# Kernel tuning notes

Hardware: AMD Instinct MI355X
Metric: run time of the kernel (lower is better)

Reference implementation:

```python
import jax, jax.numpy as jnp
import numpy as np

N = 50000      # nodes
DEG = 16       # fixed neighbor count per node -> E = N*DEG edges
F_IN = 128
F_OUT = 128


def setup_inputs() -> dict:
    key = jax.random.key(0)
    k = jax.random.split(key, 6)
    E = N * DEG
    x = jax.random.normal(k[0], (N, F_IN), dtype=jnp.float32)
    weight = jax.random.normal(k[1], (F_IN, F_OUT), dtype=jnp.float32) * (1.0 / np.sqrt(F_OUT))
    bias = jax.random.normal(k[2], (F_OUT,), dtype=jnp.float32) * (1.0 / np.sqrt(F_OUT))
    weights_mask = jax.random.normal(k[3], (2 * F_IN, F_IN), dtype=jnp.float32) * (1.0 / np.sqrt(F_IN))
    adj_vals = jax.random.uniform(k[4], (E,), dtype=jnp.float32)
    edge_src = jax.random.randint(k[5], (E,), 0, N, dtype=jnp.int32)   # neighbor ids (add_all flattened)
    edge_dst = jnp.repeat(jnp.arange(N, dtype=jnp.int32), DEG)         # center node ids
    return {"x": x, "weight": weight, "bias": bias, "weights_mask": weights_mask,
            "adj_vals": adj_vals, "edge_src": edge_src, "edge_dst": edge_dst}


def reference(x, weight, bias, weights_mask, adj_vals, edge_src, edge_dst):
    # Per-edge: concat(center, neighbor) -> mask MLP -> sigmoid (dropout omitted: eval mode)
    cen = x[edge_dst]                    # [E, F]
    nei = x[edge_src]                    # [E, F]
    cen_nei = jnp.concatenate([cen, nei], axis=1)          # [E, 2F]
    mask = jax.nn.sigmoid(cen_nei @ weights_mask)          # [E, F]
    # Weighted neighbor sum scattered back to centers, plus self feature
    agg = jax.ops.segment_sum(mask * nei, edge_dst, num_segments=N)   # [N, F]
    x_new = x + agg
    # Dense transform then spmm aggregation (adj given as edge list with values)
    support = x_new @ weight                                # [N, F_out]
    out = jax.ops.segment_sum(adj_vals[:, None] * support[edge_src], edge_dst, num_segments=N)
    return out + bias
```

## Files before the change

### kernel.cpp

```cpp
#include <hip/hip_runtime.h>
#include <stdint.h>
#include <stddef.h>


#define NNODES 50000
#define DEG    16
#define FD     128

#define NEG_LOG2E -1.44269504f

typedef __bf16 bf16x8 __attribute__((ext_vector_type(8)));
typedef short  s16x8  __attribute__((ext_vector_type(8)));
typedef float  f32x4  __attribute__((ext_vector_type(4)));
typedef float  f32x2  __attribute__((ext_vector_type(2)));

__device__ __forceinline__ short f2bf_s(float f) {
    union { float f; uint32_t u; } v; v.f = f;
    uint32_t r = v.u + 0x7fffu + ((v.u >> 16) & 1u);
    return (short)(r >> 16);
}
__device__ __forceinline__ float bflo(uint32_t u) {
    union { uint32_t u; float f; } v; v.u = u << 16;
    return v.f;
}
__device__ __forceinline__ float bfhi(uint32_t u) {
    union { uint32_t u; float f; } v; v.u = u & 0xffff0000u;
    return v.f;
}

__global__ __launch_bounds__(256) void pack_k(const float* __restrict__ wm,
                                              const float* __restrict__ w,
                                              short* __restrict__ wmb,
                                              short* __restrict__ wpack) {
    int tid = blockIdx.x * 256 + threadIdx.x;
    if (tid < 128 * 256) {
        int k = tid >> 8, c = tid & 255;
        float v = (c < 128) ? wm[k * 128 + c] : wm[(128 + k) * 128 + (c - 128)];
        int idx = (((k >> 5) * 16 + (c >> 4)) * 64 + ((k >> 3) & 3) * 16 + (c & 15)) * 8 + (k & 7);
        wmb[idx] = f2bf_s(NEG_LOG2E * v);
    }
    if (tid < 128 * 128) {
        int k = tid >> 7, n = tid & 127;
        int idx = (((k >> 5) * 8 + (n >> 4)) * 64 + ((k >> 3) & 3) * 16 + (n & 15)) * 8 + (k & 7);
        wpack[idx] = f2bf_s(w[tid]);
    }
}

__global__ __launch_bounds__(256) void zy_k(const float* __restrict__ x,
                                            const short* __restrict__ wmb,
                                            short* __restrict__ zbf,
                                            uint32_t* __restrict__ xy) {
    __shared__ float ct[16 * 260];
    const int tid = threadIdx.x, wave = tid >> 6, lane = tid & 63;
    const int q = lane >> 4, m = lane & 15;
    const int node0 = blockIdx.x * 16;

    f32x4 acc[4];
    #pragma unroll
    for (int nt = 0; nt < 4; ++nt) acc[nt] = (f32x4){0.f, 0.f, 0.f, 0.f};

    #pragma unroll
    for (int kk = 0; kk < 4; ++kk) {
        const float* rp = x + (size_t)(node0 + m) * FD + kk * 32 + q * 8;
        f32x4 lo = *reinterpret_cast<const f32x4*>(rp);
        f32x4 hi = *reinterpret_cast<const f32x4*>(rp + 4);
        bf16x8 a;
        a[0]=(__bf16)lo.x; a[1]=(__bf16)lo.y; a[2]=(__bf16)lo.z; a[3]=(__bf16)lo.w;
        a[4]=(__bf16)hi.x; a[5]=(__bf16)hi.y; a[6]=(__bf16)hi.z; a[7]=(__bf16)hi.w;
        #pragma unroll
        for (int nt = 0; nt < 4; ++nt) {
            int frag = kk * 16 + wave * 4 + nt;
            s16x8 braw = *reinterpret_cast<const s16x8*>(wmb + ((size_t)frag * 64 + lane) * 8);
            acc[nt] = __builtin_amdgcn_mfma_f32_16x16x32_bf16(a, __builtin_bit_cast(bf16x8, braw), acc[nt], 0, 0, 0);
        }
    }
    #pragma unroll
    for (int nt = 0; nt < 4; ++nt)
        #pragma unroll
        for (int i = 0; i < 4; ++i)
            ct[(q * 4 + i) * 260 + wave * 64 + nt * 16 + m] = acc[nt][i];
    __syncthreads();

    const int row = tid >> 4;
    const int c0  = (tid & 15) * 16;
    const int grow = node0 + row;
    if (c0 < 128) {
        uint32_t zo[8];
        #pragma unroll
        for (int j = 0; j < 8; ++j) {
            float v0 = ct[row * 260 + c0 + 2 * j];
            float v1 = ct[row * 260 + c0 + 2 * j + 1];
            zo[j] = (uint32_t)(uint16_t)f2bf_s(v0) | ((uint32_t)(uint16_t)f2bf_s(v1) << 16);
        }
        uint4* dst = reinterpret_cast<uint4*>(zbf + (size_t)grow * FD + c0);
        dst[0] = make_uint4(zo[0], zo[1], zo[2], zo[3]);
        dst[1] = make_uint4(zo[4], zo[5], zo[6], zo[7]);
    } else {
        const int f0 = c0 - 128;
        const float* xr = x + (size_t)grow * FD + f0;
        uint4* dst = reinterpret_cast<uint4*>(xy + (size_t)grow * FD + f0);
        #pragma unroll
        for (int v = 0; v < 4; ++v) {
            uint32_t xo[4];
            #pragma unroll
            for (int j = 0; j < 4; ++j) {
                float yv = ct[row * 260 + c0 + v * 4 + j];
                float xv = xr[v * 4 + j];
                xo[j] = (uint32_t)(uint16_t)f2bf_s(xv) | ((uint32_t)(uint16_t)f2bf_s(yv) << 16);
            }
            dst[v] = make_uint4(xo[0], xo[1], xo[2], xo[3]);
        }
    }
}

__global__ __launch_bounds__(256) void edge_k(const short* __restrict__ zbf,
                                              const uint32_t* __restrict__ xy,
                                              const int* __restrict__ esrc,
                                              const short* __restrict__ wpack,
                                              short* __restrict__ support) {
    __shared__ float xn[16 * 132];
    const int tid = threadIdx.x, wave = tid >> 6, lane = tid & 63;
    const int q = lane >> 4, m = lane & 15;
    const int node0 = blockIdx.x * 16;
    const int nu0 = __builtin_amdgcn_readfirstlane(node0 + wave * 4);

    uint2     buf[2][16];
    uint2     cr[2];
    uint32_t  zr[2];

    {
        const int* ep = esrc + nu0 * DEG;
        #pragma unroll
        for (int e = 0; e < 16; ++e)
            buf[0][e] = reinterpret_cast<const uint2*>(xy + (size_t)ep[e] * FD)[lane];
        zr[0] = reinterpret_cast<const uint32_t*>(zbf + (size_t)nu0 * FD)[lane];
        cr[0] = reinterpret_cast<const uint2*>(xy + (size_t)nu0 * FD)[lane];
    }

    #pragma unroll
    for (int mt = 0; mt < 4; ++mt) {
        const int cur = mt & 1, nxt = cur ^ 1;
        if (mt < 3) {
            const int nun = nu0 + mt + 1;
            const int* ep = esrc + nun * DEG;
            #pragma unroll
            for (int e = 0; e < 16; ++e)
                buf[nxt][e] = reinterpret_cast<const uint2*>(xy + (size_t)ep[e] * FD)[lane];
            zr[nxt] = reinterpret_cast<const uint32_t*>(zbf + (size_t)nun * FD)[lane];
            cr[nxt] = reinterpret_cast<const uint2*>(xy + (size_t)nun * FD)[lane];
        }
        const float zn0 = bflo(zr[cur]), zn1 = bfhi(zr[cur]);
        float a0a = 0.f, a0b = 0.f, a1a = 0.f, a1b = 0.f;
        #pragma unroll
        for (int e = 0; e < 16; ++e) {
            uint2 u = buf[cur][e];
            float g0 = __builtin_amdgcn_rcpf(1.f + __builtin_amdgcn_exp2f(zn0 + bfhi(u.x)));
            float g1 = __builtin_amdgcn_rcpf(1.f + __builtin_amdgcn_exp2f(zn1 + bfhi(u.y)));
            if (e & 1) { a0b += g0 * bflo(u.x); a1b += g1 * bflo(u.y); }
            else       { a0a += g0 * bflo(u.x); a1a += g1 * bflo(u.y); }
        }
        f32x2 xv;
        xv.x = bflo(cr[cur].x) + a0a + a0b;
        xv.y = bflo(cr[cur].y) + a1a + a1b;
        *reinterpret_cast<f32x2*>(&xn[(wave * 4 + mt) * 132 + 2 * lane]) = xv;
    }
    __syncthreads();

    f32x4 sacc[2];
    sacc[0] = (f32x4){0.f, 0.f, 0.f, 0.f};
    sacc[1] = (f32x4){0.f, 0.f, 0.f, 0.f};
    #pragma unroll
    for (int kk = 0; kk < 4; ++kk) {
        const float* p = &xn[m * 132 + kk * 32 + q * 8];
        bf16x8 a;
        a[0]=(__bf16)p[0]; a[1]=(__bf16)p[1]; a[2]=(__bf16)p[2]; a[3]=(__bf16)p[3];
        a[4]=(__bf16)p[4]; a[5]=(__bf16)p[5]; a[6]=(__bf16)p[6]; a[7]=(__bf16)p[7];
        #pragma unroll
        for (int t = 0; t < 2; ++t) {
            int nt = wave * 2 + t;
            s16x8 braw = *reinterpret_cast<const s16x8*>(wpack + ((size_t)(kk * 8 + nt) * 64 + lane) * 8);
            sacc[t] = __builtin_amdgcn_mfma_f32_16x16x32_bf16(a, __builtin_bit_cast(bf16x8, braw), sacc[t], 0, 0, 0);
        }
    }
    #pragma unroll
    for (int t = 0; t < 2; ++t) {
        int nt = wave * 2 + t;
        #pragma unroll
        for (int i = 0; i < 4; ++i)
            support[(size_t)(node0 + q * 4 + i) * FD + nt * 16 + m] = f2bf_s(sacc[t][i]);
    }
}

__global__ __launch_bounds__(256) void final_k(const short* __restrict__ support,
                                               const float* __restrict__ adj,
                                               const int* __restrict__ esrc,
                                               const float* __restrict__ bias,
                                               float* __restrict__ out) {
    const int tid = threadIdx.x, wave = tid >> 6, lane = tid & 63;
    const int n0 = blockIdx.x * 16 + wave * 4;
    f32x2 b = *reinterpret_cast<const f32x2*>(bias + 2 * lane);

    int nu[4];
    const int* ep[4];
    const float* ap[4];
    #pragma unroll
    for (int t = 0; t < 4; ++t) {
        nu[t] = __builtin_amdgcn_readfirstlane(n0 + t);
        ep[t] = esrc + nu[t] * DEG;
        ap[t] = adj + nu[t] * DEG;
    }
    float a0[4], a1[4];
    #pragma unroll
    for (int t = 0; t < 4; ++t) { a0[t] = b.x; a1[t] = b.y; }

    #pragma unroll
    for (int e = 0; e < 16; ++e) {
        #pragma unroll
        for (int t = 0; t < 4; ++t) {
            int s = ep[t][e];
            float w = ap[t][e];
            uint32_t u = reinterpret_cast<const uint32_t*>(support + (size_t)s * FD)[lane];
            a0[t] += w * bflo(u);
            a1[t] += w * bfhi(u);
        }
    }
    #pragma unroll
    for (int t = 0; t < 4; ++t) {
        f32x2 r; r.x = a0[t]; r.y = a1[t];
        *reinterpret_cast<f32x2*>(out + (size_t)nu[t] * FD + 2 * lane) = r;
    }
}

extern "C" void kernel_launch(void* const* d_in, const int* in_sizes, int n_in,
                              void* d_out, int out_size, void* d_ws, size_t ws_size,
                              hipStream_t stream) {
    const float* x      = (const float*)d_in[0];
    const float* weight = (const float*)d_in[1];
    const float* bias   = (const float*)d_in[2];
    const float* wm     = (const float*)d_in[3];
    const float* adj    = (const float*)d_in[4];
    const int*   esrc   = (const int*)d_in[5];

    short*    wmb     = (short*)d_ws;
    short*    wpack   = (short*)((char*)d_ws + 65536);
    short*    zbf     = (short*)((char*)d_ws + 98304);
    short*    support = (short*)((char*)d_ws + 98304 + (size_t)NNODES * FD * 2);
    uint32_t* xy      = (uint32_t*)d_out;
    float*    out     = (float*)d_out;

    pack_k <<<128,         256, 0, stream>>>(wm, weight, wmb, wpack);
    zy_k   <<<NNODES / 16, 256, 0, stream>>>(x, wmb, zbf, xy);
    edge_k <<<NNODES / 16, 256, 0, stream>>>(zbf, xy, esrc, wpack, support);
    final_k<<<NNODES / 16, 256, 0, stream>>>(support, adj, esrc, bias, out);
}
```

Baseline: 198.1 us.

## Reorder spmm before weight GEMM, store neighbor mask term in fp8

Uses linearity to aggregate x_new over neighbors first and apply the weight matrix afterwards, so the GEMM is fused into the final aggregation kernel and the intermediate support tensor disappears. The edge kernel now writes bf16 x_new and drops the in-kernel GEMM and LDS staging. The neighbor-side mask projection y is stored as fp8 in a separate array from the bf16 x, which cuts the bytes gathered per edge. Risks are lower precision in the mask logits and the extra rounding of x_new to bf16 before aggregation.

```diff
diff --git a/kernel.cpp b/kernel.cpp
--- a/kernel.cpp
+++ b/kernel.cpp
@@ -49,7 +49,8 @@
 __global__ __launch_bounds__(256) void zy_k(const float* __restrict__ x,
                                             const short* __restrict__ wmb,
                                             short* __restrict__ zbf,
-                                            uint32_t* __restrict__ xy) {
+                                            uint32_t* __restrict__ xb,
+                                            uint8_t* __restrict__ y8) {
     __shared__ float ct[16 * 260];
     const int tid = threadIdx.x, wave = tid >> 6, lane = tid & 63;
     const int q = lane >> 4, m = lane & 15;
@@ -98,71 +99,110 @@
     } else {
         const int f0 = c0 - 128;
         const float* xr = x + (size_t)grow * FD + f0;
-        uint4* dst = reinterpret_cast<uint4*>(xy + (size_t)grow * FD + f0);
-        #pragma unroll
-        for (int v = 0; v < 4; ++v) {
-            uint32_t xo[4];
-            #pragma unroll
-            for (int j = 0; j < 4; ++j) {
-                float yv = ct[row * 260 + c0 + v * 4 + j];
-                float xv = xr[v * 4 + j];
-                xo[j] = (uint32_t)(uint16_t)f2bf_s(xv) | ((uint32_t)(uint16_t)f2bf_s(yv) << 16);
-            }
-            dst[v] = make_uint4(xo[0], xo[1], xo[2], xo[3]);
-        }
+        uint32_t xo[8];
+        #pragma unroll
+        for (int j = 0; j < 8; ++j) {
+            float v0 = xr[2 * j], v1 = xr[2 * j + 1];
+            xo[j] = (uint32_t)(uint16_t)f2bf_s(v0) | ((uint32_t)(uint16_t)f2bf_s(v1) << 16);
+        }
+        uint4* xdst = reinterpret_cast<uint4*>(xb + (size_t)grow * 64 + f0 / 2);
+        xdst[0] = make_uint4(xo[0], xo[1], xo[2], xo[3]);
+        xdst[1] = make_uint4(xo[4], xo[5], xo[6], xo[7]);
+        uint32_t yo[4];
+        #pragma unroll
+        for (int g = 0; g < 4; ++g) {
+            float y0 = ct[row * 260 + c0 + 4 * g];
+            float y1 = ct[row * 260 + c0 + 4 * g + 1];
+            float y2 = ct[row * 260 + c0 + 4 * g + 2];
+            float y3 = ct[row * 260 + c0 + 4 * g + 3];
+            int u = __builtin_amdgcn_cvt_pk_fp8_f32(y0, y1, 0, false);
+            u     = __builtin_amdgcn_cvt_pk_fp8_f32(y2, y3, u, true);
+            yo[g] = (uint32_t)u;
+        }
+        *reinterpret_cast<uint4*>(y8 + (size_t)grow * 128 + f0) = make_uint4(yo[0], yo[1], yo[2], yo[3]);
     }
 }
 
 __global__ __launch_bounds__(256) void edge_k(const short* __restrict__ zbf,
-                                              const uint32_t* __restrict__ xy,
+                                              const uint32_t* __restrict__ xb,
+                                              const uint8_t* __restrict__ y8,
                                               const int* __restrict__ esrc,
-                                              const short* __restrict__ wpack,
-                                              short* __restrict__ support) {
+                                              uint32_t* __restrict__ xnb) {
+    const int tid = threadIdx.x, wave = tid >> 6, lane = tid & 63;
+    const int wn0 = blockIdx.x * 16 + wave * 4;
+
+    #pragma unroll
+    for (int pr = 0; pr < 2; ++pr) {
+        const int nuA = __builtin_amdgcn_readfirstlane(wn0 + pr * 2);
+        const int nuB = __builtin_amdgcn_readfirstlane(wn0 + pr * 2 + 1);
+        const int* epA = esrc + nuA * DEG;
+        const int* epB = esrc + nuB * DEG;
+        uint32_t zA = reinterpret_cast<const uint32_t*>(zbf + (size_t)nuA * FD)[lane];
+        uint32_t zB = reinterpret_cast<const uint32_t*>(zbf + (size_t)nuB * FD)[lane];
+        uint32_t cAw = xb[(size_t)nuA * 64 + lane];
+        uint32_t cBw = xb[(size_t)nuB * 64 + lane];
+        const float zA0 = bflo(zA), zA1 = bfhi(zA);
+        const float zB0 = bflo(zB), zB1 = bfhi(zB);
+        float aA0 = 0.f, aA1 = 0.f, bA0 = 0.f, bA1 = 0.f;
+        float aB0 = 0.f, aB1 = 0.f, bB0 = 0.f, bB1 = 0.f;
+        #pragma unroll
+        for (int e = 0; e < 16; ++e) {
+            const int sA = epA[e], sB = epB[e];
+            uint32_t xA = xb[(size_t)sA * 64 + lane];
+            uint32_t xB = xb[(size_t)sB * 64 + lane];
+            uint32_t yA = *reinterpret_cast<const uint16_t*>(y8 + (size_t)sA * 128 + 2 * lane);
+            uint32_t yB = *reinterpret_cast<const uint16_t*>(y8 + (size_t)sB * 128 + 2 * lane);
+            f32x2 pA = __builtin_amdgcn_cvt_pk_f32_fp8((int)yA, false);
+            f32x2 pB = __builtin_amdgcn_cvt_pk_f32_fp8((int)yB, false);
+            float gA0 = __builtin_amdgcn_rcpf(1.f + __builtin_amdgcn_exp2f(zA0 + pA.x));
+            float gA1 = __builtin_amdgcn_rcpf(1.f + __builtin_amdgcn_exp2f(zA1 + pA.y));
+            float gB0 = __builtin_amdgcn_rcpf(1.f + __builtin_amdgcn_exp2f(zB0 + pB.x));
+            float gB1 = __builtin_amdgcn_rcpf(1.f + __builtin_amdgcn_exp2f(zB1 + pB.y));
+            if (e & 1) { bA0 += gA0 * bflo(xA); bA1 += gA1 * bfhi(xA); bB0 += gB0 * bflo(xB); bB1 += gB1 * bfhi(xB); }
+            else       { aA0 += gA0 * bflo(xA); aA1 += gA1 * bfhi(xA); aB0 += gB0 * bflo(xB); aB1 += gB1 * bfhi(xB); }
+        }
+        float xA0 = bflo(cAw) + aA0 + bA0, xA1 = bfhi(cAw) + aA1 + bA1;
+        float xB0 = bflo(cBw) + aB0 + bB0, xB1 = bfhi(cBw) + aB1 + bB1;
+        xnb[(size_t)nuA * 64 + lane] = (uint32_t)(uint16_t)f2bf_s(xA0) | ((uint32_t)(uint16_t)f2bf_s(xA1) << 16);
+        xnb[(size_t)nuB * 64 + lane] = (uint32_t)(uint16_t)f2bf_s(xB0) | ((uint32_t)(uint16_t)f2bf_s(xB1) << 16);
+    }
+}
+
+__global__ __launch_bounds__(256) void out_k(const uint32_t* __restrict__ xnb,
+                                             const float* __restrict__ adj,
+                                             const int* __restrict__ esrc,
+                                             const short* __restrict__ wpack,
+                                             const float* __restrict__ bias,
+                                             float* __restrict__ out) {
     __shared__ float xn[16 * 132];
     const int tid = threadIdx.x, wave = tid >> 6, lane = tid & 63;
     const int q = lane >> 4, m = lane & 15;
     const int node0 = blockIdx.x * 16;
-    const int nu0 = __builtin_amdgcn_readfirstlane(node0 + wave * 4);
-
-    uint2     buf[2][16];
-    uint2     cr[2];
-    uint32_t  zr[2];
-
-    {
-        const int* ep = esrc + nu0 * DEG;
-        #pragma unroll
-        for (int e = 0; e < 16; ++e)
-            buf[0][e] = reinterpret_cast<const uint2*>(xy + (size_t)ep[e] * FD)[lane];
-        zr[0] = reinterpret_cast<const uint32_t*>(zbf + (size_t)nu0 * FD)[lane];
-        cr[0] = reinterpret_cast<const uint2*>(xy + (size_t)nu0 * FD)[lane];
-    }
-
-    #pragma unroll
-    for (int mt = 0; mt < 4; ++mt) {
-        const int cur = mt & 1, nxt = cur ^ 1;
-        if (mt < 3) {
-            const int nun = nu0 + mt + 1;
-            const int* ep = esrc + nun * DEG;
-            #pragma unroll
-            for (int e = 0; e < 16; ++e)
-                buf[nxt][e] = reinterpret_cast<const uint2*>(xy + (size_t)ep[e] * FD)[lane];
-            zr[nxt] = reinterpret_cast<const uint32_t*>(zbf + (size_t)nun * FD)[lane];
-            cr[nxt] = reinterpret_cast<const uint2*>(xy + (size_t)nun * FD)[lane];
-        }
-        const float zn0 = bflo(zr[cur]), zn1 = bfhi(zr[cur]);
-        float a0a = 0.f, a0b = 0.f, a1a = 0.f, a1b = 0.f;
+    const int wn0 = node0 + wave * 4;
+
+    #pragma unroll
+    for (int pr = 0; pr < 2; ++pr) {
+        const int nuA = __builtin_amdgcn_readfirstlane(wn0 + pr * 2);
+        const int nuB = __builtin_amdgcn_readfirstlane(wn0 + pr * 2 + 1);
+        const int* epA = esrc + nuA * DEG;
+        const int* epB = esrc + nuB * DEG;
+        const float* apA = adj + nuA * DEG;
+        const float* apB = adj + nuB * DEG;
+        float aA0 = 0.f, aA1 = 0.f, bA0 = 0.f, bA1 = 0.f;
+        float aB0 = 0.f, aB1 = 0.f, bB0 = 0.f, bB1 = 0.f;
         #pragma unroll
         for (int e = 0; e < 16; ++e) {
-            uint2 u = buf[cur][e];
-            float g0 = __builtin_amdgcn_rcpf(1.f + __builtin_amdgcn_exp2f(zn0 + bfhi(u.x)));
-            float g1 = __builtin_amdgcn_rcpf(1.f + __builtin_amdgcn_exp2f(zn1 + bfhi(u.y)));
-            if (e & 1) { a0b += g0 * bflo(u.x); a1b += g1 * bflo(u.y); }
-            else       { a0a += g0 * bflo(u.x); a1a += g1 * bflo(u.y); }
-        }
-        f32x2 xv;
-        xv.x = bflo(cr[cur].x) + a0a + a0b;
-        xv.y = bflo(cr[cur].y) + a1a + a1b;
-        *reinterpret_cast<f32x2*>(&xn[(wave * 4 + mt) * 132 + 2 * lane]) = xv;
+            uint32_t uA = xnb[(size_t)epA[e] * 64 + lane];
+            uint32_t uB = xnb[(size_t)epB[e] * 64 + lane];
+            float wA = apA[e], wB = apB[e];
+            if (e & 1) { bA0 += wA * bflo(uA); bA1 += wA * bfhi(uA); bB0 += wB * bflo(uB); bB1 += wB * bfhi(uB); }
+            else       { aA0 += wA * bflo(uA); aA1 += wA * bfhi(uA); aB0 += wB * bflo(uB); aB1 += wB * bfhi(uB); }
+        }
+        const int rA = wave * 4 + pr * 2, rB = rA + 1;
+        f32x2 tA; tA.x = aA0 + bA0; tA.y = aA1 + bA1;
+        f32x2 tB; tB.x = aB0 + bB0; tB.y = aB1 + bB1;
+        *reinterpret_cast<f32x2*>(&xn[rA * 132 + 2 * lane]) = tA;
+        *reinterpret_cast<f32x2*>(&xn[rB * 132 + 2 * lane]) = tB;
     }
     __syncthreads();
 
@@ -184,50 +224,11 @@
     }
     #pragma unroll
     for (int t = 0; t < 2; ++t) {
-        int nt = wave * 2 + t;
+        const int f = (wave * 2 + t) * 16 + m;
+        const float bv = bias[f];
         #pragma unroll
         for (int i = 0; i < 4; ++i)
-            support[(size_t)(node0 + q * 4 + i) * FD + nt * 16 + m] = f2bf_s(sacc[t][i]);
-    }
-}
-
-__global__ __launch_bounds__(256) void final_k(const short* __restrict__ support,
-                                               const float* __restrict__ adj,
-                                               const int* __restrict__ esrc,
-                                               const float* __restrict__ bias,
-                                               float* __restrict__ out) {
-    const int tid = threadIdx.x, wave = tid >> 6, lane = tid & 63;
-    const int n0 = blockIdx.x * 16 + wave * 4;
-    f32x2 b = *reinterpret_cast<const f32x2*>(bias + 2 * lane);
-
-    int nu[4];
-    const int* ep[4];
-    const float* ap[4];
-    #pragma unroll
-    for (int t = 0; t < 4; ++t) {
-        nu[t] = __builtin_amdgcn_readfirstlane(n0 + t);
-        ep[t] = esrc + nu[t] * DEG;
-        ap[t] = adj + nu[t] * DEG;
-    }
-    float a0[4], a1[4];
-    #pragma unroll
-    for (int t = 0; t < 4; ++t) { a0[t] = b.x; a1[t] = b.y; }
-
-    #pragma unroll
-    for (int e = 0; e < 16; ++e) {
-        #pragma unroll
-        for (int t = 0; t < 4; ++t) {
-            int s = ep[t][e];
-            float w = ap[t][e];
-            uint32_t u = reinterpret_cast<const uint32_t*>(support + (size_t)s * FD)[lane];
-            a0[t] += w * bflo(u);
-            a1[t] += w * bfhi(u);
-        }
-    }
-    #pragma unroll
-    for (int t = 0; t < 4; ++t) {
-        f32x2 r; r.x = a0[t]; r.y = a1[t];
-        *reinterpret_cast<f32x2*>(out + (size_t)nu[t] * FD + 2 * lane) = r;
+            out[(size_t)(node0 + q * 4 + i) * FD + f] = sacc[t][i] + bv;
     }
 }
 
@@ -241,15 +242,16 @@
     const float* adj    = (const float*)d_in[4];
     const int*   esrc   = (const int*)d_in[5];
 
-    short*    wmb     = (short*)d_ws;
-    short*    wpack   = (short*)((char*)d_ws + 65536);
-    short*    zbf     = (short*)((char*)d_ws + 98304);
-    short*    support = (short*)((char*)d_ws + 98304 + (size_t)NNODES * FD * 2);
-    uint32_t* xy      = (uint32_t*)d_out;
-    float*    out     = (float*)d_out;
+    short*    wmb   = (short*)d_ws;
+    short*    wpack = (short*)((char*)d_ws + 65536);
+    short*    zbf   = (short*)((char*)d_ws + 98304);
+    uint32_t* xnb   = (uint32_t*)((char*)d_ws + 98304 + (size_t)NNODES * FD * 2);
+    uint32_t* xb    = (uint32_t*)d_out;
+    uint8_t*  y8    = (uint8_t*)d_out + (size_t)NNODES * FD * 2;
+    float*    out   = (float*)d_out;
 
     pack_k <<<128,         256, 0, stream>>>(wm, weight, wmb, wpack);
-    zy_k   <<<NNODES / 16, 256, 0, stream>>>(x, wmb, zbf, xy);
-    edge_k <<<NNODES / 16, 256, 0, stream>>>(zbf, xy, esrc, wpack, support);
-    final_k<<<NNODES / 16, 256, 0, stream>>>(support, adj, esrc, bias, out);
-}
+    zy_k   <<<NNODES / 16, 256, 0, stream>>>(x, wmb, zbf, xb, y8);
+    edge_k <<<NNODES / 16, 256, 0, stream>>>(zbf, xb, y8, esrc, xnb);
+    out_k  <<<NNODES / 16, 256, 0, stream>>>(xnb, adj, esrc, wpack, bias, out);
+}
```

Result: faster. 180.3 us (-9.0%).
